# Kernel tuning notes

Measured on AMD Instinct MI355X. Metric: run time of the kernel, lower is better.

Reference implementation:

```python
import jax, jax.numpy as jnp
import numpy as np

NUM_NODES = 20000
HIDDEN = 64
NUM_EDGES = 640000
LEAK = 0.2  # PyG GATConv negative_slope default


def gat_conv(x, w, a_src, a_dst, b, src, dst, n):
    # x: [N, F_in]; w: [F_in, H*C]; a_src/a_dst: [H, C]; edges j=src -> i=dst
    H, C = a_src.shape
    xe = (x @ w).reshape(n, H, C)                         # [N, H, C]
    es = jnp.einsum('nhc,hc->nh', xe, a_src)              # alpha_src per node
    ed = jnp.einsum('nhc,hc->nh', xe, a_dst)              # alpha_dst per node
    e = jax.nn.leaky_relu(es[src] + ed[dst], LEAK)        # [E, H] edge logits
    # segment softmax over each destination's incoming edges
    m = jax.ops.segment_max(e, dst, num_segments=n)
    p = jnp.exp(e - m[dst])
    s = jax.ops.segment_sum(p, dst, num_segments=n)
    alpha = p / s[dst]                                    # [E, H]
    out = jax.ops.segment_sum(alpha[:, :, None] * xe[src], dst, num_segments=n)
    return out.reshape(n, H * C) + b                      # concat heads + bias


def setup_inputs() -> dict:
    key = jax.random.key(0)
    ks = jax.random.split(key, 16)
    B, S, N, Hd = 4, 12, NUM_NODES, HIDDEN
    sc = 0.1
    inp = {}
    inp['x'] = jax.random.normal(ks[0], (B, S, N), jnp.float32)
    inp['edge_index'] = jax.random.randint(ks[1], (2, NUM_EDGES), 0, N, jnp.int32)
    inp['proj_w'] = jax.random.normal(ks[2], (S, Hd), jnp.float32) * sc
    inp['proj_b'] = jnp.zeros((Hd,), jnp.float32)
    inp['gat0_w'] = jax.random.normal(ks[3], (Hd, Hd), jnp.float32) * sc
    inp['gat0_asrc'] = jax.random.normal(ks[4], (8, 8), jnp.float32) * sc
    inp['gat0_adst'] = jax.random.normal(ks[5], (8, 8), jnp.float32) * sc
    inp['gat0_b'] = jnp.zeros((Hd,), jnp.float32)
    inp['gat1_w'] = jax.random.normal(ks[6], (Hd, Hd), jnp.float32) * sc
    inp['gat1_asrc'] = jax.random.normal(ks[7], (8, 8), jnp.float32) * sc
    inp['gat1_adst'] = jax.random.normal(ks[8], (8, 8), jnp.float32) * sc
    inp['gat1_b'] = jnp.zeros((Hd,), jnp.float32)
    inp['gat2_w'] = jax.random.normal(ks[9], (Hd, Hd), jnp.float32) * sc
    inp['gat2_asrc'] = jax.random.normal(ks[10], (1, Hd), jnp.float32) * sc
    inp['gat2_adst'] = jax.random.normal(ks[11], (1, Hd), jnp.float32) * sc
    inp['gat2_b'] = jnp.zeros((Hd,), jnp.float32)
    inp['conv_w'] = jax.random.normal(ks[12], (Hd, Hd, 3), jnp.float32) * sc
    inp['conv_b'] = jnp.zeros((Hd,), jnp.float32)
    inp['out_w'] = jax.random.normal(ks[13], (Hd, 3), jnp.float32) * sc
    inp['out_b'] = jnp.zeros((3,), jnp.float32)
    return inp


def reference(x, edge_index, proj_w, proj_b,
              gat0_w, gat0_asrc, gat0_adst, gat0_b,
              gat1_w, gat1_asrc, gat1_adst, gat1_b,
              gat2_w, gat2_asrc, gat2_adst, gat2_b,
              conv_w, conv_b, out_w, out_b):
    B, S, N = x.shape
    # PyG GATConv add_self_loops=True
    loops = jnp.arange(N, dtype=edge_index.dtype)
    src = jnp.concatenate([edge_index[0], loops])
    dst = jnp.concatenate([edge_index[1], loops])
    h = jnp.transpose(x, (0, 2, 1)) @ proj_w + proj_b     # [B, N, Hd]
    layers = [(gat0_w, gat0_asrc, gat0_adst, gat0_b),
              (gat1_w, gat1_asrc, gat1_adst, gat1_b),
              (gat2_w, gat2_asrc, gat2_adst, gat2_b)]
    for i, (w, asr, ads, b) in enumerate(layers):
        h = jax.vmap(lambda hb: gat_conv(hb, w, asr, ads, b, src, dst, N))(h)
        if i < len(layers) - 1:
            h = jax.nn.elu(h)                             # dropout is identity in eval
    hc = jnp.transpose(h, (0, 2, 1))                      # [B, Hd, N]
    hc = jax.lax.conv_general_dilated(hc, conv_w, (1,), ((1, 1),),
                                      dimension_numbers=('NCH', 'OIH', 'NCH'))
    hc = jax.nn.relu(hc + conv_b[None, :, None])
    h = jnp.transpose(hc, (0, 2, 1)) @ out_w + out_b      # [B, N, pred]
    return jnp.transpose(h, (0, 2, 1))                    # [B, pred, N]
```

## Files before the change

kernel.cpp:

```cpp
#include <hip/hip_runtime.h>
#include <math.h>

constexpr int B  = 4;
constexpr int S  = 12;
constexpr int N  = 20000;
constexpr int HD = 64;
constexpr int E0 = 640000;
constexpr int EL = E0 + N;
constexpr int BN = B * N;
constexpr int CAP = 128;

__global__ void scatter_kernel(const int* __restrict__ ei, int* __restrict__ cnt,
                               int* __restrict__ perm) {
    int e = blockIdx.x * blockDim.x + threadIdx.x;
    if (e >= EL) return;
    int s, d;
    if (e < E0) { s = ei[e]; d = ei[E0 + e]; }
    else        { s = e - E0; d = s; }
    int pos = atomicAdd(&cnt[d], 1) & (CAP - 1);
    perm[d * CAP + pos] = s;
}

__global__ void tw_kernel(const float* __restrict__ cw, float* __restrict__ cwD) {
    int i = blockIdx.x * blockDim.x + threadIdx.x;
    if (i >= HD * HD * 3) return;
    int o = i / (HD * 3), rem = i % (HD * 3), c = rem / 3, dt = rem % 3;
    cwD[dt * (HD * HD) + c * HD + o] = cw[i];
}

constexpr int GT = 64;

template<int H>
__global__ __launch_bounds__(256, 4)
void gemm_attn_kernel(const float* __restrict__ hin, const float* __restrict__ w,
                      const float* __restrict__ asrc, const float* __restrict__ adst,
                      float* __restrict__ xe, float* __restrict__ es, float* __restrict__ ed) {
    __shared__ float tile[GT * HD];
    int base = blockIdx.x * GT;
    for (int i = threadIdx.x; i < GT * (HD / 4); i += 256)
        ((float4*)tile)[i] = ((const float4*)(hin + (size_t)base * HD))[i];
    int lane = threadIdx.x & 63;
    float wres[HD];
    #pragma unroll
    for (int c = 0; c < HD; ++c) wres[c] = w[c * HD + lane];
    float as_ = asrc[lane], ad_ = adst[lane];
    __syncthreads();
    int wvid = threadIdx.x >> 6;
    for (int j = wvid * 16; j < wvid * 16 + 16; ++j) {
        int t = base + j;
        float acc = 0.f;
        #pragma unroll
        for (int cq = 0; cq < 16; ++cq) {
            float4 r = ((const float4*)tile)[j * 16 + cq];
            acc = fmaf(r.x, wres[4 * cq + 0], acc);
            acc = fmaf(r.y, wres[4 * cq + 1], acc);
            acc = fmaf(r.z, wres[4 * cq + 2], acc);
            acc = fmaf(r.w, wres[4 * cq + 3], acc);
        }
        xe[(size_t)t * HD + lane] = acc;
        float t0 = acc * as_, t1 = acc * ad_;
        if (H == 8) {
            #pragma unroll
            for (int m = 1; m < 8; m <<= 1) {
                t0 += __shfl_xor(t0, m, 64);
                t1 += __shfl_xor(t1, m, 64);
            }
            if ((lane & 7) == 0) {
                es[t * 8 + (lane >> 3)] = t0;
                ed[t * 8 + (lane >> 3)] = t1;
            }
        } else {
            #pragma unroll
            for (int m = 1; m < 64; m <<= 1) {
                t0 += __shfl_xor(t0, m, 64);
                t1 += __shfl_xor(t1, m, 64);
            }
            if (lane == 0) { es[t] = t0; ed[t] = t1; }
        }
    }
}

__global__ __launch_bounds__(256, 4)
void fused0_kernel(const float* __restrict__ x, const float* __restrict__ pw,
                   const float* __restrict__ pb, const float* __restrict__ w,
                   const float* __restrict__ asrc, const float* __restrict__ adst,
                   float* __restrict__ xe, float* __restrict__ es, float* __restrict__ ed) {
    __shared__ float tile[GT * HD];
    __shared__ float xt[S * GT];
    int base = blockIdx.x * GT;
    for (int i = threadIdx.x; i < S * GT; i += 256) {
        int s = i >> 6, nl = i & 63;
        int t = base + nl, bb = t / N, n = t - bb * N;
        xt[i] = x[(bb * S + s) * N + n];
    }
    int lane = threadIdx.x & 63;
    float wres[HD];
    #pragma unroll
    for (int c = 0; c < HD; ++c) wres[c] = w[c * HD + lane];
    float pwres[S];
    #pragma unroll
    for (int s = 0; s < S; ++s) pwres[s] = pw[s * HD + lane];
    float pbv = pb[lane];
    float as_ = asrc[lane], ad_ = adst[lane];
    __syncthreads();
    int wvid = threadIdx.x >> 6;
    for (int j = wvid * 16; j < wvid * 16 + 16; ++j) {
        float hl = pbv;
        #pragma unroll
        for (int s = 0; s < S; ++s)
            hl = fmaf(xt[s * GT + j], pwres[s], hl);
        tile[j * HD + lane] = hl;
    }
    for (int j = wvid * 16; j < wvid * 16 + 16; ++j) {
        int t = base + j;
        float acc = 0.f;
        #pragma unroll
        for (int cq = 0; cq < 16; ++cq) {
            float4 r = ((const float4*)tile)[j * 16 + cq];
            acc = fmaf(r.x, wres[4 * cq + 0], acc);
            acc = fmaf(r.y, wres[4 * cq + 1], acc);
            acc = fmaf(r.z, wres[4 * cq + 2], acc);
            acc = fmaf(r.w, wres[4 * cq + 3], acc);
        }
        xe[(size_t)t * HD + lane] = acc;
        float t0 = acc * as_, t1 = acc * ad_;
        #pragma unroll
        for (int m = 1; m < 8; m <<= 1) {
            t0 += __shfl_xor(t0, m, 64);
            t1 += __shfl_xor(t1, m, 64);
        }
        if ((lane & 7) == 0) {
            es[t * 8 + (lane >> 3)] = t0;
            ed[t * 8 + (lane >> 3)] = t1;
        }
    }
}

template<int H, bool DO_ELU>
__global__ __launch_bounds__(256, 8)
void agg_kernel(const float* __restrict__ xe, const float* __restrict__ es,
                const float* __restrict__ ed, const int* __restrict__ cnt,
                const int* __restrict__ perm, const float* __restrict__ bias,
                float* __restrict__ hout) {
    int g = blockIdx.x;
    int bb   = (g & 7) >> 1;
    int idx  = (g >> 3) * 2 + (g & 1);
    int node = idx * 4 + (threadIdx.x >> 6);
    int lane  = threadIdx.x & 63;
    int group = lane >> 4;
    int c4    = lane & 15;
    int deg = cnt[node];
    int baseE = node * CAP;
    int h = (H == 8) ? (c4 >> 1) : 0;
    const float*  es_b = es + bb * (N * H);
    const float4* xe4  = (const float4*)(xe + bb * (N * HD));
    float edv = ed[(bb * N + node) * H + h];
    float4 acc = {0.f, 0.f, 0.f, 0.f};
    float ssum = 0.f;
    #pragma unroll 2
    for (int jb = 0; jb < deg; jb += 4) {
        int j = jb + group;
        bool valid = (j < deg);
        int src = perm[baseE + (valid ? j : 0)];
        float e = es_b[src * H + h] + edv;
        e = fmaxf(e, 0.2f * e);
        float p = valid ? __expf(e) : 0.f;
        ssum += p;
        float4 xv = xe4[src * 16 + c4];
        acc.x = fmaf(p, xv.x, acc.x);
        acc.y = fmaf(p, xv.y, acc.y);
        acc.z = fmaf(p, xv.z, acc.z);
        acc.w = fmaf(p, xv.w, acc.w);
    }
    #pragma unroll
    for (int m = 16; m < 64; m <<= 1) {
        acc.x += __shfl_xor(acc.x, m, 64);
        acc.y += __shfl_xor(acc.y, m, 64);
        acc.z += __shfl_xor(acc.z, m, 64);
        acc.w += __shfl_xor(acc.w, m, 64);
        ssum  += __shfl_xor(ssum,  m, 64);
    }
    if (lane < 16) {
        float inv = 1.f / ssum;
        const float4* b4 = (const float4*)bias;
        float4 bv = b4[c4];
        float4 r;
        r.x = acc.x * inv + bv.x;
        r.y = acc.y * inv + bv.y;
        r.z = acc.z * inv + bv.z;
        r.w = acc.w * inv + bv.w;
        if (DO_ELU) {
            r.x = (r.x > 0.f) ? r.x : expm1f(r.x);
            r.y = (r.y > 0.f) ? r.y : expm1f(r.y);
            r.z = (r.z > 0.f) ? r.z : expm1f(r.z);
            r.w = (r.w > 0.f) ? r.w : expm1f(r.w);
        }
        ((float4*)hout)[(bb * N + node) * 16 + c4] = r;
    }
}

constexpr int CN = 64;
__global__ __launch_bounds__(256, 2)
void conv_out_kernel(const float* __restrict__ h, const float* __restrict__ cwD,
                     const float* __restrict__ cb, const float* __restrict__ ow,
                     const float* __restrict__ ob, float* __restrict__ out) {
    __shared__ float tile[(CN + 2) * HD];
    __shared__ float part[CN * HD];
    int bb = blockIdx.y;
    int base = blockIdx.x * CN;
    for (int i = threadIdx.x; i < (CN + 2) * (HD / 4); i += 256) {
        int row = i >> 4, q = i & 15;
        int m = base - 1 + row;
        float4 v = {0.f, 0.f, 0.f, 0.f};
        if (m >= 0 && m < N) v = ((const float4*)(h + ((size_t)bb * N + m) * HD))[q];
        ((float4*)tile)[i] = v;
    }
    int lane = threadIdx.x & 63;
    int wvid = threadIdx.x >> 6;
    float cbv = cb[lane];
    float ow0 = ow[lane * 3 + 0], ow1 = ow[lane * 3 + 1], ow2 = ow[lane * 3 + 2];
    float ob0 = ob[0], ob1 = ob[1], ob2 = ob[2];
    #pragma unroll
    for (int j = 0; j < 16; ++j)
        part[(wvid * 16 + j) * HD + lane] = cbv;
    __syncthreads();
    #pragma unroll 1
    for (int dt = 0; dt < 3; ++dt) {
        float wres[HD];
        #pragma unroll
        for (int c = 0; c < HD; ++c) wres[c] = cwD[dt * (HD * HD) + c * HD + lane];
        #pragma unroll 1
        for (int j = 0; j < 16; ++j) {
            const float4* rp = (const float4*)(tile + (wvid * 16 + j + dt) * HD);
            float a = 0.f;
            #pragma unroll
            for (int cq = 0; cq < 16; ++cq) {
                float4 r = rp[cq];
                a = fmaf(r.x, wres[4 * cq + 0], a);
                a = fmaf(r.y, wres[4 * cq + 1], a);
                a = fmaf(r.z, wres[4 * cq + 2], a);
                a = fmaf(r.w, wres[4 * cq + 3], a);
            }
            part[(wvid * 16 + j) * HD + lane] += a;
        }
    }
    #pragma unroll 1
    for (int j = 0; j < 16; ++j) {
        float v = fmaxf(part[(wvid * 16 + j) * HD + lane], 0.f);
        float t0 = v * ow0, t1 = v * ow1, t2 = v * ow2;
        #pragma unroll
        for (int m = 1; m < 64; m <<= 1) {
            t0 += __shfl_xor(t0, m, 64);
            t1 += __shfl_xor(t1, m, 64);
            t2 += __shfl_xor(t2, m, 64);
        }
        int n = base + wvid * 16 + j;
        if (lane < 3 && n < N) {
            float r = (lane == 0) ? t0 + ob0 : (lane == 1) ? t1 + ob1 : t2 + ob2;
            out[(size_t)bb * 3 * N + lane * N + n] = r;
        }
    }
}

extern "C" void kernel_launch(void* const* d_in, const int* in_sizes, int n_in,
                              void* d_out, int out_size, void* d_ws, size_t ws_size,
                              hipStream_t stream) {
    const float* x      = (const float*)d_in[0];
    const int*   ei     = (const int*)  d_in[1];
    const float* proj_w = (const float*)d_in[2];
    const float* proj_b = (const float*)d_in[3];
    const float* g_w [3] = {(const float*)d_in[4], (const float*)d_in[8],  (const float*)d_in[12]};
    const float* g_as[3] = {(const float*)d_in[5], (const float*)d_in[9],  (const float*)d_in[13]};
    const float* g_ad[3] = {(const float*)d_in[6], (const float*)d_in[10], (const float*)d_in[14]};
    const float* g_b [3] = {(const float*)d_in[7], (const float*)d_in[11], (const float*)d_in[15]};
    const float* conv_w = (const float*)d_in[16];
    const float* conv_b = (const float*)d_in[17];
    const float* out_w  = (const float*)d_in[18];
    const float* out_b  = (const float*)d_in[19];
    float* out = (float*)d_out;

    float* bufA = (float*)d_ws;
    float* bufX = bufA + (size_t)BN * HD;
    float* es   = bufX + (size_t)BN * HD;
    float* ed   = es   + (size_t)BN * 8;
    int* cnt  = (int*)(ed + (size_t)BN * 8);
    int* perm = cnt + N;
    float* cwD = (float*)(perm + (size_t)N * CAP);

    const int TB = 256;
    const int gE = (EL + TB - 1) / TB;

    hipMemsetAsync(cnt, 0, N * sizeof(int), stream);
    scatter_kernel<<<gE, TB, 0, stream>>>(ei, cnt, perm);

    tw_kernel<<<(HD * HD * 3 + TB - 1) / TB, TB, 0, stream>>>(conv_w, cwD);

    fused0_kernel<<<BN / GT, TB, 0, stream>>>(x, proj_w, proj_b, g_w[0], g_as[0], g_ad[0],
                                              bufX, es, ed);
    agg_kernel<8, true><<<BN / 4, TB, 0, stream>>>(bufX, es, ed, cnt, perm, g_b[0], bufA);

    gemm_attn_kernel<8><<<BN / GT, TB, 0, stream>>>(bufA, g_w[1], g_as[1], g_ad[1], bufX, es, ed);
    agg_kernel<8, true><<<BN / 4, TB, 0, stream>>>(bufX, es, ed, cnt, perm, g_b[1], bufA);

    gemm_attn_kernel<1><<<BN / GT, TB, 0, stream>>>(bufA, g_w[2], g_as[2], g_ad[2], bufX, es, ed);
    agg_kernel<1, false><<<BN / 4, TB, 0, stream>>>(bufX, es, ed, cnt, perm, g_b[2], bufA);

    conv_out_kernel<<<dim3((N + CN - 1) / CN, B), TB, 0, stream>>>(bufA, cwD, conv_b, out_w, out_b, out);
}
```

Baseline: 497.8 us.

## Keep conv accumulators in registers and share tile row reads across taps

The conv+output kernel drops its shared-memory partial-sum buffer and keeps the 16 per-wave accumulators in registers. It also loads two tap weight sets together so each LDS tile row is read once for taps 0 and 1, then makes a second pass for tap 2. Separately, the GAT aggregation edge loop's unroll factor goes from 2 to 4. Holding 128 weight registers plus 16 accumulators raises register pressure and may cut occupancy or cause spills.

```diff
diff --git a/kernel.cpp b/kernel.cpp
--- a/kernel.cpp
+++ b/kernel.cpp
@@ -157,7 +157,7 @@
     float edv = ed[(bb * N + node) * H + h];
     float4 acc = {0.f, 0.f, 0.f, 0.f};
     float ssum = 0.f;
-    #pragma unroll 2
+    #pragma unroll 4
     for (int jb = 0; jb < deg; jb += 4) {
         int j = jb + group;
         bool valid = (j < deg);
@@ -205,7 +205,6 @@
                      const float* __restrict__ cb, const float* __restrict__ ow,
                      const float* __restrict__ ob, float* __restrict__ out) {
     __shared__ float tile[(CN + 2) * HD];
-    __shared__ float part[CN * HD];
     int bb = blockIdx.y;
     int base = blockIdx.x * CN;
     for (int i = threadIdx.x; i < (CN + 2) * (HD / 4); i += 256) {
@@ -217,36 +216,58 @@
     }
     int lane = threadIdx.x & 63;
     int wvid = threadIdx.x >> 6;
+    int nb = wvid * 16;
     float cbv = cb[lane];
     float ow0 = ow[lane * 3 + 0], ow1 = ow[lane * 3 + 1], ow2 = ow[lane * 3 + 2];
     float ob0 = ob[0], ob1 = ob[1], ob2 = ob[2];
-    #pragma unroll
-    for (int j = 0; j < 16; ++j)
-        part[(wvid * 16 + j) * HD + lane] = cbv;
+    float acc[16];
+    #pragma unroll
+    for (int j = 0; j < 16; ++j) acc[j] = cbv;
+    float w0[HD], w1[HD];
+    #pragma unroll
+    for (int c = 0; c < HD; ++c) w0[c] = cwD[c * HD + lane];
+    #pragma unroll
+    for (int c = 0; c < HD; ++c) w1[c] = cwD[HD * HD + c * HD + lane];
     __syncthreads();
-    #pragma unroll 1
-    for (int dt = 0; dt < 3; ++dt) {
-        float wres[HD];
-        #pragma unroll
-        for (int c = 0; c < HD; ++c) wres[c] = cwD[dt * (HD * HD) + c * HD + lane];
-        #pragma unroll 1
-        for (int j = 0; j < 16; ++j) {
-            const float4* rp = (const float4*)(tile + (wvid * 16 + j + dt) * HD);
-            float a = 0.f;
-            #pragma unroll
-            for (int cq = 0; cq < 16; ++cq) {
-                float4 r = rp[cq];
-                a = fmaf(r.x, wres[4 * cq + 0], a);
-                a = fmaf(r.y, wres[4 * cq + 1], a);
-                a = fmaf(r.z, wres[4 * cq + 2], a);
-                a = fmaf(r.w, wres[4 * cq + 3], a);
-            }
-            part[(wvid * 16 + j) * HD + lane] += a;
-        }
-    }
-    #pragma unroll 1
+    #pragma unroll
+    for (int r = 0; r <= 16; ++r) {
+        const float4* rp = (const float4*)(tile + (nb + r) * HD);
+        float a0 = 0.f, a1 = 0.f;
+        #pragma unroll
+        for (int cq = 0; cq < 16; ++cq) {
+            float4 rv = rp[cq];
+            a0 = fmaf(rv.x, w0[4 * cq + 0], a0);
+            a0 = fmaf(rv.y, w0[4 * cq + 1], a0);
+            a0 = fmaf(rv.z, w0[4 * cq + 2], a0);
+            a0 = fmaf(rv.w, w0[4 * cq + 3], a0);
+            a1 = fmaf(rv.x, w1[4 * cq + 0], a1);
+            a1 = fmaf(rv.y, w1[4 * cq + 1], a1);
+            a1 = fmaf(rv.z, w1[4 * cq + 2], a1);
+            a1 = fmaf(rv.w, w1[4 * cq + 3], a1);
+        }
+        if (r <= 15) acc[r] += a0;
+        if (r >= 1)  acc[r - 1] += a1;
+    }
+    float w2[HD];
+    #pragma unroll
+    for (int c = 0; c < HD; ++c) w2[c] = cwD[2 * HD * HD + c * HD + lane];
+    #pragma unroll
+    for (int r = 2; r <= 17; ++r) {
+        const float4* rp = (const float4*)(tile + (nb + r) * HD);
+        float a2 = 0.f;
+        #pragma unroll
+        for (int cq = 0; cq < 16; ++cq) {
+            float4 rv = rp[cq];
+            a2 = fmaf(rv.x, w2[4 * cq + 0], a2);
+            a2 = fmaf(rv.y, w2[4 * cq + 1], a2);
+            a2 = fmaf(rv.z, w2[4 * cq + 2], a2);
+            a2 = fmaf(rv.w, w2[4 * cq + 3], a2);
+        }
+        acc[r - 2] += a2;
+    }
+    #pragma unroll
     for (int j = 0; j < 16; ++j) {
-        float v = fmaxf(part[(wvid * 16 + j) * HD + lane], 0.f);
+        float v = fmaxf(acc[j], 0.f);
         float t0 = v * ow0, t1 = v * ow1, t2 = v * ow2;
         #pragma unroll
         for (int m = 1; m < 64; m <<= 1) {
@@ -254,7 +275,7 @@
             t1 += __shfl_xor(t1, m, 64);
             t2 += __shfl_xor(t2, m, 64);
         }
-        int n = base + wvid * 16 + j;
+        int n = base + nb + j;
         if (lane < 3 && n < N) {
             float r = (lane == 0) ? t0 + ob0 : (lane == 1) ? t1 + ob1 : t2 + ob2;
             out[(size_t)bb * 3 * N + lane * N + n] = r;
```

Result: slower. 1.932 ms (+288.2%).
